# Kernel tuning notes

Hardware: AMD Instinct MI355X
Metric: run time of the kernel (lower is better)

## Reference

```python
import jax, jax.numpy as jnp
import numpy as np


def setup_inputs() -> dict:
    key = jax.random.key(0)
    kq, kk, kv = jax.random.split(key, 3)
    B, T, D = 8, 2048, 512
    return {
        "query": jax.random.normal(kq, (B, T, D), dtype=jnp.float32),
        "key": jax.random.normal(kk, (B, T, D), dtype=jnp.float32),
        "value": jax.random.normal(kv, (B, T, D), dtype=jnp.float32),
        "mask_future": 1,
    }


def reference(query, key, value, mask_future):
    # scores[b, t, s] = sum_d Q[b, t, d] * K[b, s, d]
    scores = jnp.einsum('btd,bsd->bts', query, key)
    dk = jnp.sqrt(jnp.asarray(key.shape[-1], dtype=jnp.float32))
    if mask_future:
        # Faithful to the TF code: band_part(ones, 0, -1) keeps the upper
        # triangle INCLUDING the diagonal; mask = 1 - (1 + 1e9) * upper,
        # applied MULTIPLICATIVELY to the raw scores (quirky but intentional).
        T, S = scores.shape[-2], scores.shape[-1]
        upper = jnp.triu(jnp.ones((T, S), dtype=scores.dtype), k=0)
        mult = 1.0 - (1.0 + 1e9) * upper  # 1 below diag, -1e9 on/above diag
        scores = scores * mult
    x = jax.nn.softmax(scores / dk, axis=-1)
    return jnp.einsum('bts,bsd->btd', x, value)
```

## Files before the change

kernel.cpp:

```cpp
#include <hip/hip_runtime.h>
#include <math.h>

#define BATCH 8
#define SEQ   2048
#define DIM   512
#define NCH   16
#define CHW   128
#define CAP   512

typedef unsigned int u32;
typedef unsigned long long u64;
typedef _Float16 h2  __attribute__((ext_vector_type(2)));
typedef _Float16 h8  __attribute__((ext_vector_type(8)));
typedef float    f4  __attribute__((ext_vector_type(4)));
typedef u32      u4v __attribute__((ext_vector_type(4)));

#define MFMA16(a,b,c) __builtin_amdgcn_mfma_f32_16x16x32_f16((a),(b),(c),0,0,0)

struct HL { u32 hi, lo; };
__device__ __forceinline__ HL split2t(float a, float b) {
    _Float16 ha = (_Float16)a, hb = (_Float16)b;
    h2 th; th[0] = ha; th[1] = hb;
    h2 tl; tl[0] = (_Float16)(a - (float)ha); tl[1] = (_Float16)(b - (float)hb);
    HL r; r.hi = __builtin_bit_cast(u32, th); r.lo = __builtin_bit_cast(u32, tl);
    return r;
}
__device__ __forceinline__ u32 fkey(float f) {
    u32 v = __builtin_bit_cast(u32, f);
    return (v & 0x80000000u) ? ~v : (v | 0x80000000u);
}

__global__ __launch_bounds__(256, 4)
void prep_kernel(const float* __restrict__ Q, const float* __restrict__ K,
                 u32* __restrict__ Qh, u32* __restrict__ Ql,
                 u32* __restrict__ Kh, u32* __restrict__ Kl)
{
    const int lane = threadIdx.x & 63;
    const int lx   = lane & 15, lg = lane >> 4;
    if (blockIdx.x < 1024) {
        const int b    = blockIdx.x >> 7;
        const int g16  = blockIdx.x & 127;
        const int tq   = threadIdx.x >> 6;
        const float* src0 = Q + ((size_t)(b * SEQ + g16 * 16 + lx)) * DIM + 8 * lg;
        #pragma unroll
        for (int p = 0; p < 4; p++) {
            const int t = p * 4 + tq;
            const float* s = src0 + 32 * t;
            const f4 r0 = *(const f4*)(s);
            const f4 r1 = *(const f4*)(s + 4);
            const HL p0 = split2t(r0[0], r0[1]);
            const HL p1 = split2t(r0[2], r0[3]);
            const HL p2 = split2t(r1[0], r1[1]);
            const HL p3 = split2t(r1[2], r1[3]);
            u4v vh = {p0.hi, p1.hi, p2.hi, p3.hi};
            u4v vl = {p0.lo, p1.lo, p2.lo, p3.lo};
            const size_t off = (((size_t)(b * 128 + g16) * 16 + t) * 256) + (size_t)lane * 4;
            *(u4v*)(Qh + off) = vh;
            *(u4v*)(Ql + off) = vl;
        }
    } else {
        const int blk  = blockIdx.x - 1024;
        const int b    = blk >> 8;
        const int st   = (blk >> 4) & 15;
        const int t    = blk & 15;
        const int nq   = threadIdx.x >> 6;
        #pragma unroll
        for (int p = 0; p < 2; p++) {
            const int nt = p * 4 + nq;
            const float* s = K + ((size_t)(b * SEQ + 128 * st + 16 * nt + lx)) * DIM + 32 * t + 8 * lg;
            const f4 r0 = *(const f4*)(s);
            const f4 r1 = *(const f4*)(s + 4);
            const HL p0 = split2t(r0[0], r0[1]);
            const HL p1 = split2t(r0[2], r0[3]);
            const HL p2 = split2t(r1[0], r1[1]);
            const HL p3 = split2t(r1[2], r1[3]);
            u4v vh = {p0.hi, p1.hi, p2.hi, p3.hi};
            u4v vl = {p0.lo, p1.lo, p2.lo, p3.lo};
            const size_t off = ((((size_t)(b * 16 + st) * 16 + t) * 8 + nt) * 256) + (size_t)lane * 4;
            *(u4v*)(Kh + off) = vh;
            *(u4v*)(Kl + off) = vl;
        }
    }
}

__global__ __launch_bounds__(256, 2)
void argmin4_kernel(const u32* __restrict__ Qh, const u32* __restrict__ Ql,
                    const u32* __restrict__ Kh, const u32* __restrict__ Kl,
                    const int* __restrict__ mfp, u64* __restrict__ keys)
{
    if (mfp[0] == 0) return;

    const int tid  = threadIdx.x;
    const int b    = blockIdx.x & 7;
    int rem        = blockIdx.x >> 3;
    const int w    = tid >> 6;
    const int lane = tid & 63, lx = lane & 15, lg = lane >> 4;

    int g = 0;
    while (rem >= 16 - g) { rem -= 16 - g; g++; }
    const int st   = g + rem;
    const int s0   = 128 * st;
    const int g16b = 8 * g + 2 * w;
    const int m0   = 128 * g + 32 * w;

    const f4 fz = {0.f, 0.f, 0.f, 0.f};
    f4 sa[2][8];
    #pragma unroll
    for (int rg = 0; rg < 2; rg++)
        #pragma unroll
        for (int nt = 0; nt < 8; nt++) sa[rg][nt] = fz;

    const size_t qoff = ((size_t)(b * 128 + g16b) * 16) * 256 + (size_t)lane * 4;
    const size_t koff = ((size_t)(b * 16 + st) * 128) * 256 + (size_t)lane * 4;

    #pragma unroll
    for (int t = 0; t < 16; t++) {
        h8 ah[2], al[2];
        #pragma unroll
        for (int rg = 0; rg < 2; rg++) {
            ah[rg] = __builtin_bit_cast(h8, *(const u4v*)(Qh + qoff + (size_t)(rg * 16 + t) * 256));
            al[rg] = __builtin_bit_cast(h8, *(const u4v*)(Ql + qoff + (size_t)(rg * 16 + t) * 256));
        }
        h8 kh[8], kl[8];
        #pragma unroll
        for (int nt = 0; nt < 8; nt++) {
            kh[nt] = __builtin_bit_cast(h8, *(const u4v*)(Kh + koff + (size_t)(t * 8 + nt) * 256));
            kl[nt] = __builtin_bit_cast(h8, *(const u4v*)(Kl + koff + (size_t)(t * 8 + nt) * 256));
        }
        __builtin_amdgcn_s_setprio(1);
        #pragma unroll
        for (int nt = 0; nt < 8; nt++) {
            #pragma unroll
            for (int rg = 0; rg < 2; rg++) {
                sa[rg][nt] = MFMA16(ah[rg], kh[nt], sa[rg][nt]);
                sa[rg][nt] = MFMA16(ah[rg], kl[nt], sa[rg][nt]);
                sa[rg][nt] = MFMA16(al[rg], kh[nt], sa[rg][nt]);
            }
        }
        __builtin_amdgcn_s_setprio(0);
    }

    #pragma unroll
    for (int rg = 0; rg < 2; rg++) {
        #pragma unroll
        for (int nt = 0; nt < 8; nt++)
            #pragma unroll
            for (int r = 0; r < 4; r++) {
                float s = sa[rg][nt][r];
                sa[rg][nt][r] = (s == s) ? s : 0.0f;
            }
        #pragma unroll
        for (int r = 0; r < 4; r++) {
            const int tg = m0 + 16 * rg + 4 * lg + r;
            float mv = INFINITY; int mi = -1;
            #pragma unroll
            for (int nt = 0; nt < 8; nt++) {
                const int sg = s0 + 16 * nt + lx;
                const float v = sa[rg][nt][r];
                if (sg >= tg && v < mv) { mv = v; mi = sg; }
            }
            #pragma unroll
            for (int off = 1; off < 16; off <<= 1) {
                const float ov = __shfl_xor(mv, off);
                const int   oi = __shfl_xor(mi, off);
                if (ov < mv || (ov == mv && oi >= 0 && (mi < 0 || oi < mi))) { mv = ov; mi = oi; }
            }
            if (lx == 0 && mi >= 0) {
                const u64 pk = ((u64)fkey(mv) << 32) | (u32)mi;
                atomicMin(&keys[(size_t)b * SEQ + tg], pk);
            }
        }
    }
}

__global__ __launch_bounds__(512, 2)
void argmin_lds_kernel(const float* __restrict__ Q, const float* __restrict__ K,
                       const int* __restrict__ mfp, u64* __restrict__ ws)
{
    if (mfp[0] == 0) return;
    __shared__ u32 KTh[2][128][32];
    __shared__ u32 KTl[2][128][32];
    __shared__ float sx[128][68];

    const int tid  = threadIdx.x;
    const int w    = tid >> 6, wp = w & 3, h = w >> 2;
    const int lane = tid & 63, lx = lane & 15, lg = lane >> 4;

    int j = blockIdx.x;
    const int b = j / 272; j -= b * 272;
    int mg = 0;
    while (true) { const int n = 16 - (mg >> 1); if (j < n) break; j -= n; mg++; }
    const int m0 = mg * 64;
    const int s0 = (m0 & ~127) + 128 * j;

    const float* __restrict__ Qb = Q + (size_t)b * SEQ * DIM;
    const float* __restrict__ Kb = K + (size_t)b * SEQ * DIM;
    const int krow = (tid >> 1) & 127;
    const int ksc  = tid & 1;

    h8 qh[8], ql[8];
    {
        const float* qrowp = Qb + (size_t)(m0 + 16 * wp + lx) * DIM;
        #pragma unroll
        for (int t = 0; t < 8; t++) {
            float bufv[8];
            *(f4*)&bufv[0] = *(const f4*)(qrowp + 256 * h + 32 * t + 8 * lg);
            *(f4*)&bufv[4] = *(const f4*)(qrowp + 256 * h + 32 * t + 8 * lg + 4);
            u4v uh, ul;
            #pragma unroll
            for (int p = 0; p < 4; p++) {
                const HL hl = split2t(bufv[2*p], bufv[2*p+1]);
                uh[p] = hl.hi; ul[p] = hl.lo;
            }
            qh[t] = __builtin_bit_cast(h8, uh);
            ql[t] = __builtin_bit_cast(h8, ul);
        }
    }
    const f4 fz = {0.f, 0.f, 0.f, 0.f};
    f4 sa[8];
    #pragma unroll
    for (int nt = 0; nt < 8; nt++) sa[nt] = fz;

    f4 kreg[8];
    #pragma unroll
    for (int c = 0; c < 8; c++)
        kreg[c] = *(const f4*)(Kb + (size_t)(s0 + krow) * DIM + 256 * h + 32 * ksc + 4 * c);

    #pragma unroll
    for (int i = 0; i < 4; i++) {
        if (i) __syncthreads();
        {
            u32 HH[16], LL[16];
            #pragma unroll
            for (int c = 0; c < 8; c++) {
                const HL e0 = split2t(kreg[c][0], kreg[c][1]);
                const HL e1 = split2t(kreg[c][2], kreg[c][3]);
                HH[2*c] = e0.hi;   LL[2*c] = e0.lo;
                HH[2*c+1] = e1.hi; LL[2*c+1] = e1.lo;
            }
            #pragma unroll
            for (int qd = 0; qd < 4; qd++) {
                const int gp = ((4 * ksc + qd) ^ (krow & 7)) * 4;
                u4v vh = {HH[4*qd], HH[4*qd+1], HH[4*qd+2], HH[4*qd+3]};
                u4v vl = {LL[4*qd], LL[4*qd+1], LL[4*qd+2], LL[4*qd+3]};
                *(u4v*)&KTh[h][krow][gp] = vh;
                *(u4v*)&KTl[h][krow][gp] = vl;
            }
        }
        __syncthreads();
        if (i < 3) {
            #pragma unroll
            for (int c = 0; c < 8; c++)
                kreg[c] = *(const f4*)(Kb + (size_t)(s0 + krow) * DIM
                                       + 256 * h + 64 * (i + 1) + 32 * ksc + 4 * c);
        }
        __builtin_amdgcn_s_setprio(1);
        #pragma unroll
        for (int tl = 0; tl < 2; tl++) {
            const int t = 2 * i + tl;
            #pragma unroll
            for (int nt = 0; nt < 8; nt++) {
                const int s  = 16 * nt + lx;
                const int gp = ((4 * tl + lg) ^ (s & 7)) * 4;
                const h8 kh = __builtin_bit_cast(h8, *(const u4v*)&KTh[h][s][gp]);
                const h8 kl = __builtin_bit_cast(h8, *(const u4v*)&KTl[h][s][gp]);
                sa[nt] = MFMA16(qh[t], kh, sa[nt]);
                sa[nt] = MFMA16(qh[t], kl, sa[nt]);
                sa[nt] = MFMA16(ql[t], kh, sa[nt]);
            }
        }
        __builtin_amdgcn_s_setprio(0);
    }

    if (h == 0) {
        #pragma unroll
        for (int nt = 0; nt < 8; nt++)
            *(f4*)&sx[16 * nt + lx][16 * wp + 4 * lg] = sa[nt];
    }
    __syncthreads();
    if (h == 1) {
        #pragma unroll
        for (int nt = 0; nt < 8; nt++) {
            const f4 part = *(const f4*)&sx[16 * nt + lx][16 * wp + 4 * lg];
            #pragma unroll
            for (int r = 0; r < 4; r++) {
                float s = sa[nt][r] + part[r];
                sa[nt][r] = (s == s) ? s : 0.0f;
            }
        }
        #pragma unroll
        for (int r = 0; r < 4; r++) {
            const int tg = m0 + 16 * wp + 4 * lg + r;
            float mv = INFINITY; int mi = -1;
            #pragma unroll
            for (int nt = 0; nt < 8; nt++) {
                const int sg = s0 + 16 * nt + lx;
                const float v = sa[nt][r];
                if (sg >= tg && v < mv) { mv = v; mi = sg; }
            }
            #pragma unroll
            for (int off = 1; off < 16; off <<= 1) {
                const float ov = __shfl_xor(mv, off);
                const int   oi = __shfl_xor(mi, off);
                if (ov < mv || (ov == mv && oi >= 0 && (mi < 0 || oi < mi))) { mv = ov; mi = oi; }
            }
            if (lx == 0 && mi >= 0) {
                const u64 pk = ((u64)fkey(mv) << 32) | (u32)mi;
                atomicMin(&ws[(size_t)b * SEQ + tg], pk);
            }
        }
    }
}

__global__ __launch_bounds__(512, 2)
void gather_kernel(const float* __restrict__ V, const u64* __restrict__ keys,
                   u32* __restrict__ cnt, u32* __restrict__ list,
                   float* __restrict__ Out)
{
    const int tid  = threadIdx.x;
    const int w    = tid >> 6;
    const int lane = tid & 63;
    const int b    = blockIdx.x >> 5;
    const int m0   = (blockIdx.x & 31) * 64;

    const float* __restrict__ Vb = V + (size_t)b * SEQ * DIM;
    float* __restrict__ Ob = Out + (size_t)b * SEQ * DIM;

    #pragma unroll
    for (int rr = 0; rr < 8; rr++) {
        const int tg = m0 + 8 * w + rr;
        const u64 pk = keys[(size_t)b * SEQ + tg];
        const u32 key = (u32)(pk >> 32);
        if (key < 0x80000000u) {
            const int ss = (int)(pk & 0xFFFFFFFFu);
            #pragma unroll
            for (int it = 0; it < 2; it++) {
                const int col = 256 * it + 4 * lane;
                *(f4*)(Ob + (size_t)tg * DIM + col) = *(const f4*)(Vb + (size_t)ss * DIM + col);
            }
        } else if (lane == 0) {
            const u32 p = atomicAdd(cnt, 1u);
            list[p] = ((u32)b << 16) | (u32)tg;
        }
    }
}

__global__ __launch_bounds__(512, 2)
void fb_part_kernel(const float* __restrict__ Q, const float* __restrict__ K,
                    const float* __restrict__ V, const int* __restrict__ mfp,
                    const u32* __restrict__ cnt, const u32* __restrict__ list,
                    float2* __restrict__ meta, float* __restrict__ partials)
{
    __shared__ float qrow[DIM];
    __shared__ float zpart[4][CHW];
    __shared__ float zs[CHW];
    __shared__ float zp[CHW];
    __shared__ f4    pacc[4][128];
    __shared__ float red2[2];

    const int tid = threadIdx.x;
    const int mf  = mfp[0];
    const float dk = 22.627416997969522f;

    const int n  = (int)cnt[0];
    const int nw = min(n * NCH, CAP);

    for (int wi = blockIdx.x; wi < nw; wi += gridDim.x) {
        const int ridx  = wi >> 4;
        const int chunk = wi & 15;
        const u32 e  = list[ridx];
        const int b  = (int)(e >> 16);
        const int tg = (int)(e & 0xFFFFu);

        const float* __restrict__ Qb = Q + (size_t)b * SEQ * DIM;
        const float* __restrict__ Kb = K + (size_t)b * SEQ * DIM;
        const float* __restrict__ Vb = V + (size_t)b * SEQ * DIM;

        if (tid < 128) *(f4*)&qrow[4 * tid] = *(const f4*)(Qb + (size_t)tg * DIM + 4 * tid);
        __syncthreads();
        {
            const int jj   = tid & 127;
            const int dseg = tid >> 7;
            const int col  = chunk * CHW + jj;
            const float* kr = Kb + (size_t)col * DIM + 128 * dseg;
            float acc = 0.f;
            #pragma unroll 8
            for (int d4 = 0; d4 < 32; d4++) {
                const f4 q = *(const f4*)&qrow[4 * (32 * dseg + d4)];
                const f4 k = *(const f4*)(kr + 4 * d4);
                acc += q[0]*k[0] + q[1]*k[1] + q[2]*k[2] + q[3]*k[3];
            }
            zpart[dseg][jj] = acc;
        }
        __syncthreads();
        if (tid < 128) {
            const int col = chunk * CHW + tid;
            float z = zpart[0][tid] + zpart[1][tid] + zpart[2][tid] + zpart[3][tid];
            const float mult = (mf && col >= tg) ? -1.0e9f : 1.0f;
            zs[tid] = z * mult / dk;
        }
        __syncthreads();
        if (tid < 64) {
            float m = fmaxf(zs[tid], zs[tid + 64]);
            #pragma unroll
            for (int off = 1; off < 64; off <<= 1) m = fmaxf(m, __shfl_xor(m, off));
            if (tid == 0) red2[0] = m;
        }
        __syncthreads();
        const float M = red2[0];
        if (tid < 128) zp[tid] = expf(zs[tid] - M);
        __syncthreads();
        if (tid < 64) {
            float s = zp[tid] + zp[tid + 64];
            #pragma unroll
            for (int off = 1; off < 64; off <<= 1) s += __shfl_xor(s, off);
            if (tid == 0) red2[1] = s;
        }
        {
            const int dq   = tid & 127;
            const int sseg = tid >> 7;
            f4 acc = {0.f, 0.f, 0.f, 0.f};
            const int sb = chunk * CHW + 32 * sseg;
            #pragma unroll 8
            for (int s = 0; s < 32; s++)
                acc += zp[32 * sseg + s] * *(const f4*)(Vb + (size_t)(sb + s) * DIM + 4 * dq);
            pacc[sseg][dq] = acc;
        }
        __syncthreads();
        if (tid < 128) {
            const f4 nc = pacc[0][tid] + pacc[1][tid] + pacc[2][tid] + pacc[3][tid];
            *(f4*)&partials[(size_t)wi * DIM + 4 * tid] = nc;
        }
        if (tid == 0) meta[wi] = make_float2(M, red2[1]);
        __syncthreads();
    }
}

__global__ __launch_bounds__(512, 2)
void fb_combine_kernel(const float* __restrict__ Q, const float* __restrict__ K,
                       const float* __restrict__ V, const int* __restrict__ mfp,
                       const u32* __restrict__ cnt, const u32* __restrict__ list,
                       const float2* __restrict__ meta, const float* __restrict__ partials,
                       float* __restrict__ Out)
{
    __shared__ float qrow[DIM];
    __shared__ float zrow[SEQ];
    __shared__ float red[8];
    __shared__ f4    pacc[4][128];

    const int tid  = threadIdx.x;
    const int w    = tid >> 6;
    const int lane = tid & 63;
    const int mf   = mfp[0];
    const float dk = 22.627416997969522f;

    const int n = (int)cnt[0];
    for (int idx = blockIdx.x; idx < n; idx += gridDim.x) {
        const u32 e  = list[idx];
        const int b  = (int)(e >> 16);
        const int tg = (int)(e & 0xFFFFu);
        float* __restrict__ Ob = Out + (size_t)b * SEQ * DIM;

        if (idx < CAP / NCH) {
            float M = -INFINITY;
            #pragma unroll
            for (int c = 0; c < NCH; c++) M = fmaxf(M, meta[idx * NCH + c].x);
            float L = 0.f, o = 0.f;
            #pragma unroll
            for (int c = 0; c < NCH; c++) {
                const float2 mc = meta[idx * NCH + c];
                const float fct = expf(mc.x - M);
                L += mc.y * fct;
                o += partials[(size_t)(idx * NCH + c) * DIM + tid] * fct;
            }
            Ob[(size_t)tg * DIM + tid] = o / L;
        } else {
            const float* __restrict__ Qb = Q + (size_t)b * SEQ * DIM;
            const float* __restrict__ Kb = K + (size_t)b * SEQ * DIM;
            const float* __restrict__ Vb = V + (size_t)b * SEQ * DIM;
            if (tid < 128) *(f4*)&qrow[4 * tid] = *(const f4*)(Qb + (size_t)tg * DIM + 4 * tid);
            __syncthreads();
            float z4[4];
            #pragma unroll
            for (int c4 = 0; c4 < 4; c4++) {
                const int col = tid + 512 * c4;
                const float* kr = Kb + (size_t)col * DIM;
                float acc = 0.f;
                #pragma unroll 4
                for (int d4 = 0; d4 < 128; d4++) {
                    const f4 q = *(const f4*)&qrow[4 * d4];
                    const f4 k = *(const f4*)(kr + 4 * d4);
                    acc += q[0]*k[0] + q[1]*k[1] + q[2]*k[2] + q[3]*k[3];
                }
                const float mult = (mf && col >= tg) ? -1.0e9f : 1.0f;
                z4[c4] = acc * mult / dk;
            }
            float lm = fmaxf(fmaxf(z4[0], z4[1]), fmaxf(z4[2], z4[3]));
            #pragma unroll
            for (int off = 1; off < 64; off <<= 1) lm = fmaxf(lm, __shfl_xor(lm, off));
            if (lane == 0) red[w] = lm;
            __syncthreads();
            float M = red[0];
            #pragma unroll
            for (int i = 1; i < 8; i++) M = fmaxf(M, red[i]);
            float ls = 0.f;
            #pragma unroll
            for (int c4 = 0; c4 < 4; c4++) {
                const float p = expf(z4[c4] - M);
                zrow[tid + 512 * c4] = p;
                ls += p;
            }
            #pragma unroll
            for (int off = 1; off < 64; off <<= 1) ls += __shfl_xor(ls, off);
            __syncthreads();
            if (lane == 0) red[w] = ls;
            __syncthreads();
            float L = 0.f;
            #pragma unroll
            for (int i = 0; i < 8; i++) L += red[i];
            const int dq = tid & 127;
            const int sq = tid >> 7;
            f4 acc = {0.f, 0.f, 0.f, 0.f};
            const int sbeg = 512 * sq;
            #pragma unroll 8
            for (int s = 0; s < 512; s++)
                acc += zrow[sbeg + s] * *(const f4*)(Vb + (size_t)(sbeg + s) * DIM + 4 * dq);
            pacc[sq][dq] = acc;
            __syncthreads();
            if (tid < 128) {
                f4 r = pacc[0][tid] + pacc[1][tid] + pacc[2][tid] + pacc[3][tid];
                const float il = 1.0f / L;
                r[0] *= il; r[1] *= il; r[2] *= il; r[3] *= il;
                *(f4*)(Ob + (size_t)tg * DIM + 4 * tid) = r;
            }
            __syncthreads();
        }
    }
}

extern "C" void kernel_launch(void* const* d_in, const int* in_sizes, int n_in,
                              void* d_out, int out_size, void* d_ws, size_t ws_size,
                              hipStream_t stream) {
    const float* Q  = (const float*)d_in[0];
    const float* K  = (const float*)d_in[1];
    const float* V  = (const float*)d_in[2];
    const int*   mf = (const int*)d_in[3];
    float* O = (float*)d_out;

    char* wsb = (char*)d_ws;
    u64*    keys     = (u64*)wsb;
    u32*    cnt      = (u32*)(wsb + 131072);
    u32*    list     = (u32*)(wsb + 131072 + 256);
    float2* meta     = (float2*)(wsb + 131072 + 256 + 65536);
    float*  partials = (float*)(wsb + 131072 + 256 + 65536 + 8192);

    const size_t SPLIT_OFF = 1310720;
    const size_t ARR = (size_t)BATCH * SEQ * 256 * 4;
    u32* Qh = (u32*)(wsb + SPLIT_OFF);
    u32* Ql = (u32*)(wsb + SPLIT_OFF + ARR);
    u32* Kh = (u32*)(wsb + SPLIT_OFF + 2 * ARR);
    u32* Kl = (u32*)(wsb + SPLIT_OFF + 3 * ARR);
    const bool big_ws = ws_size >= SPLIT_OFF + 4 * ARR;

    hipMemsetAsync(keys, 0xFF, (size_t)BATCH * SEQ * sizeof(u64), stream);
    hipMemsetAsync(cnt, 0, sizeof(u32), stream);

    if (big_ws) {
        prep_kernel<<<dim3(3072), dim3(256), 0, stream>>>(Q, K, Qh, Ql, Kh, Kl);
        argmin4_kernel<<<dim3(1088), dim3(256), 0, stream>>>(Qh, Ql, Kh, Kl, mf, keys);
    } else {
        argmin_lds_kernel<<<dim3(BATCH * 272), dim3(512), 0, stream>>>(Q, K, mf, keys);
    }
    gather_kernel<<<dim3(BATCH * (SEQ / 64)), dim3(512), 0, stream>>>(V, keys, cnt, list, O);
    fb_part_kernel<<<dim3(512), dim3(512), 0, stream>>>(Q, K, V, mf, cnt, list, meta, partials);
    fb_combine_kernel<<<dim3(128), dim3(512), 0, stream>>>(Q, K, V, mf, cnt, list, meta, partials, O);
}
```

Before: 129.4 us.

## Stage K tiles into LDS with triple-buffered async loads shared across waves

The argmin kernel now loads K hi/lo fragments once per block into a triple-buffered LDS ring with global_load_lds, so the four waves share them instead of each reading the same K from global memory. Loads run two steps ahead, and Q fragments are double-buffered in registers with prefetch. This is meant to cut redundant global K traffic and hide load latency behind the MFMAs. In exchange it adds a barrier per step, a hand-written vmcnt wait whose count must match the number of outstanding loads, and 48KB of LDS per block, which may reduce occupancy.

```diff
diff --git a/kernel.cpp b/kernel.cpp
--- a/kernel.cpp
+++ b/kernel.cpp
@@ -28,6 +28,11 @@
 __device__ __forceinline__ u32 fkey(float f) {
     u32 v = __builtin_bit_cast(u32, f);
     return (v & 0x80000000u) ? ~v : (v | 0x80000000u);
+}
+__device__ __forceinline__ void gload_lds16(const u32* gsrc, u32* ldst) {
+    __builtin_amdgcn_global_load_lds(
+        (const __attribute__((address_space(1))) void*)gsrc,
+        (__attribute__((address_space(3))) void*)ldst, 16, 0, 0);
 }
 
 __global__ __launch_bounds__(256, 4)
@@ -84,11 +89,13 @@
 }
 
 __global__ __launch_bounds__(256, 2)
-void argmin4_kernel(const u32* __restrict__ Qh, const u32* __restrict__ Ql,
+void argmin5_kernel(const u32* __restrict__ Qh, const u32* __restrict__ Ql,
                     const u32* __restrict__ Kh, const u32* __restrict__ Kl,
                     const int* __restrict__ mfp, u64* __restrict__ keys)
 {
     if (mfp[0] == 0) return;
+
+    __shared__ u32 Kbuf[3][16][256];
 
     const int tid  = threadIdx.x;
     const int b    = blockIdx.x & 7;
@@ -103,6 +110,20 @@
     const int g16b = 8 * g + 2 * w;
     const int m0   = 128 * g + 32 * w;
 
+    const size_t qoff  = ((size_t)(b * 128 + g16b) * 16) * 256 + (size_t)lane * 4;
+    const size_t koffu = ((size_t)(b * 16 + st) * 128) * 256;
+
+    auto STAGE = [&](int t) {
+        #pragma unroll
+        for (int c4 = 0; c4 < 4; c4++) {
+            const int c  = 4 * w + c4;
+            const int nt = c & 7;
+            const u32* src = ((c < 8) ? Kh : Kl) + koffu
+                             + (size_t)(t * 8 + nt) * 256 + (size_t)lane * 4;
+            gload_lds16(src, &Kbuf[t % 3][c][0]);
+        }
+    };
+
     const f4 fz = {0.f, 0.f, 0.f, 0.f};
     f4 sa[2][8];
     #pragma unroll
@@ -110,31 +131,41 @@
         #pragma unroll
         for (int nt = 0; nt < 8; nt++) sa[rg][nt] = fz;
 
-    const size_t qoff = ((size_t)(b * 128 + g16b) * 16) * 256 + (size_t)lane * 4;
-    const size_t koff = ((size_t)(b * 16 + st) * 128) * 256 + (size_t)lane * 4;
+    h8 qhr[2][2], qlr[2][2];
+
+    STAGE(0);
+    STAGE(1);
+    #pragma unroll
+    for (int rg = 0; rg < 2; rg++) {
+        qhr[0][rg] = __builtin_bit_cast(h8, *(const u4v*)(Qh + qoff + (size_t)(rg * 16) * 256));
+        qlr[0][rg] = __builtin_bit_cast(h8, *(const u4v*)(Ql + qoff + (size_t)(rg * 16) * 256));
+    }
 
     #pragma unroll
     for (int t = 0; t < 16; t++) {
-        h8 ah[2], al[2];
-        #pragma unroll
-        for (int rg = 0; rg < 2; rg++) {
-            ah[rg] = __builtin_bit_cast(h8, *(const u4v*)(Qh + qoff + (size_t)(rg * 16 + t) * 256));
-            al[rg] = __builtin_bit_cast(h8, *(const u4v*)(Ql + qoff + (size_t)(rg * 16 + t) * 256));
-        }
-        h8 kh[8], kl[8];
+        asm volatile("s_waitcnt vmcnt(8)" ::: "memory");
+        __builtin_amdgcn_s_barrier();
+        asm volatile("" ::: "memory");
+        if (t < 14) STAGE(t + 2);
+        if (t < 15) {
+            #pragma unroll
+            for (int rg = 0; rg < 2; rg++) {
+                qhr[(t + 1) & 1][rg] = __builtin_bit_cast(h8,
+                    *(const u4v*)(Qh + qoff + (size_t)(rg * 16 + t + 1) * 256));
+                qlr[(t + 1) & 1][rg] = __builtin_bit_cast(h8,
+                    *(const u4v*)(Ql + qoff + (size_t)(rg * 16 + t + 1) * 256));
+            }
+        }
+        __builtin_amdgcn_s_setprio(1);
         #pragma unroll
         for (int nt = 0; nt < 8; nt++) {
-            kh[nt] = __builtin_bit_cast(h8, *(const u4v*)(Kh + koff + (size_t)(t * 8 + nt) * 256));
-            kl[nt] = __builtin_bit_cast(h8, *(const u4v*)(Kl + koff + (size_t)(t * 8 + nt) * 256));
-        }
-        __builtin_amdgcn_s_setprio(1);
-        #pragma unroll
-        for (int nt = 0; nt < 8; nt++) {
+            const h8 kh = __builtin_bit_cast(h8, *(const u4v*)&Kbuf[t % 3][nt][4 * lane]);
+            const h8 kl = __builtin_bit_cast(h8, *(const u4v*)&Kbuf[t % 3][8 + nt][4 * lane]);
             #pragma unroll
             for (int rg = 0; rg < 2; rg++) {
-                sa[rg][nt] = MFMA16(ah[rg], kh[nt], sa[rg][nt]);
-                sa[rg][nt] = MFMA16(ah[rg], kl[nt], sa[rg][nt]);
-                sa[rg][nt] = MFMA16(al[rg], kh[nt], sa[rg][nt]);
+                sa[rg][nt] = MFMA16(qhr[t & 1][rg], kh, sa[rg][nt]);
+                sa[rg][nt] = MFMA16(qhr[t & 1][rg], kl, sa[rg][nt]);
+                sa[rg][nt] = MFMA16(qlr[t & 1][rg], kh, sa[rg][nt]);
             }
         }
         __builtin_amdgcn_s_setprio(0);
@@ -567,7 +598,7 @@
 
     if (big_ws) {
         prep_kernel<<<dim3(3072), dim3(256), 0, stream>>>(Q, K, Qh, Ql, Kh, Kl);
-        argmin4_kernel<<<dim3(1088), dim3(256), 0, stream>>>(Qh, Ql, Kh, Kl, mf, keys);
+        argmin5_kernel<<<dim3(1088), dim3(256), 0, stream>>>(Qh, Ql, Kh, Kl, mf, keys);
     } else {
         argmin_lds_kernel<<<dim3(BATCH * 272), dim3(512), 0, stream>>>(Q, K, mf, keys);
     }
```

Measured after the change: 122.4 us. -5.4%, faster.
